# Kernel optimization log

Hardware: AMD Instinct MI355X
Metric: run time of the kernel (lower is better)

## Reference

```python
import jax, jax.numpy as jnp
import numpy as np

EPS = 1e-6
WEIGHTS = (1.0, 1.0, 1.0)  # (w_t, w_v, w_a)


def setup_inputs() -> dict:
    key = jax.random.key(0)
    k1, k2 = jax.random.split(key)
    B = 512
    similarity_cube = jax.random.normal(k1, (B, B, B), dtype=jnp.float32)
    target = jax.random.normal(k2, (B, 1), dtype=jnp.float32)
    return {"similarity_cube": similarity_cube, "target": target}


def reference(similarity_cube, target):
    # dataset == 'mosi' branch; reduction == 'mean'; weights == (1,1,1)
    # classes: round(target), >=0 -> 3, <0 -> -3 (never 0, so the eq-with-
    # intersection trick reduces to a pure 3-way class-equality mask)
    c = jnp.where(jnp.round(target[:, 0]) >= 0.0, 3.0, -3.0)  # (B,)
    # mask[i, j, k] = (c[j] == c[k]) & (c[j] == c[i])
    mask = ((c[None, :, None] == c[None, None, :])
            & (c[None, :, None] == c[:, None, None])).astype(similarity_cube.dtype)

    def axis_loss(axis):
        # masked NLL over one axis of the cube; denominators clamped at eps
        ls = jax.nn.log_softmax(similarity_cube, axis=axis)
        num = -jnp.sum(ls * mask, axis=axis)
        den = jnp.maximum(jnp.sum(mask, axis=axis), EPS)
        return num / den  # (B, B)

    # loss_t: softmax over dim 1 (transpose(1,2).view) -> per-(i,k)
    # loss_v: softmax over dim 2 (plain view)          -> per-(i,j)
    # loss_a: softmax over dim 0 (permute(1,2,0).view) -> per-(j,k)
    # all three are (B,B) row-major flattenings, so elementwise add matches torch
    loss = (WEIGHTS[0] * axis_loss(1)
            + WEIGHTS[1] * axis_loss(2)
            + WEIGHTS[2] * axis_loss(0))
    return jnp.mean(loss)
```

## Files before the change

kernel.cpp:

```cpp
#include <hip/hip_runtime.h>
#include <math.h>

#define Bn 512


__global__ void prep_kernel(const float* __restrict__ target,
                            int* __restrict__ cls,
                            int* __restrict__ nplus,
                            float* __restrict__ acc) {
    __shared__ int cnt;
    const int t = threadIdx.x;
    if (t == 0) cnt = 0;
    __syncthreads();
    const int c = (rintf(target[t]) >= 0.0f) ? 1 : 0;
    cls[t] = c;
    atomicAdd(&cnt, c);
    __syncthreads();
    if (t == 0) { *nplus = cnt; *acc = 0.0f; }
}

__global__ __launch_bounds__(256) void conloss_main(
    const float* __restrict__ cube,
    const int* __restrict__ cls,
    const int* __restrict__ nplus_p,
    float* __restrict__ acc)
{
    __shared__ int   sc[Bn];
    __shared__ float sE[4][Bn];
    __shared__ float sS[4][Bn];
    __shared__ float sred[256];

    const int tid = threadIdx.x;
    for (int t = tid; t < Bn; t += 256) sc[t] = cls[t];
    __syncthreads();
    const int np = *nplus_p;
    const int bid = blockIdx.x;
    float total = 0.0f;

    if (bid < Bn) {
        const int i = bid;
        const int ci = sc[i];
        const float inv_ng = 1.0f / (float)(ci ? np : (Bn - np));
        const int wave = tid >> 6;
        const int lane = tid & 63;
        const float* slice = cube + (size_t)i * (size_t)(Bn * Bn);
        const int ka = 4 * lane;
        const int kb = 256 + 4 * lane;

        float4 km_a, km_b;
        km_a.x = (sc[ka+0] == ci) ? 1.0f : 0.0f;
        km_a.y = (sc[ka+1] == ci) ? 1.0f : 0.0f;
        km_a.z = (sc[ka+2] == ci) ? 1.0f : 0.0f;
        km_a.w = (sc[ka+3] == ci) ? 1.0f : 0.0f;
        km_b.x = (sc[kb+0] == ci) ? 1.0f : 0.0f;
        km_b.y = (sc[kb+1] == ci) ? 1.0f : 0.0f;
        km_b.z = (sc[kb+2] == ci) ? 1.0f : 0.0f;
        km_b.w = (sc[kb+3] == ci) ? 1.0f : 0.0f;

        float4 cE_a = make_float4(0.f,0.f,0.f,0.f), cE_b = make_float4(0.f,0.f,0.f,0.f);
        float4 cS_a = make_float4(0.f,0.f,0.f,0.f), cS_b = make_float4(0.f,0.f,0.f,0.f);

        for (int j = wave; j < Bn; j += 4) {
            const float* row = slice + (size_t)j * Bn;
            const float4 xa = *(const float4*)(row + ka);
            const float4 xb = *(const float4*)(row + kb);
            float4 ea, eb;
            ea.x = __expf(xa.x); ea.y = __expf(xa.y); ea.z = __expf(xa.z); ea.w = __expf(xa.w);
            eb.x = __expf(xb.x); eb.y = __expf(xb.y); eb.z = __expf(xb.z); eb.w = __expf(xb.w);

            const float jm = (sc[j] == ci) ? 1.0f : 0.0f;
            cE_a.x += ea.x; cE_a.y += ea.y; cE_a.z += ea.z; cE_a.w += ea.w;
            cE_b.x += eb.x; cE_b.y += eb.y; cE_b.z += eb.z; cE_b.w += eb.w;
            cS_a.x += jm * xa.x; cS_a.y += jm * xa.y; cS_a.z += jm * xa.z; cS_a.w += jm * xa.w;
            cS_b.x += jm * xb.x; cS_b.y += jm * xb.y; cS_b.z += jm * xb.z; cS_b.w += jm * xb.w;

            float rE = ((ea.x + ea.y) + (ea.z + ea.w)) + ((eb.x + eb.y) + (eb.z + eb.w));
            float rS = km_a.x * xa.x + km_a.y * xa.y + km_a.z * xa.z + km_a.w * xa.w
                     + km_b.x * xb.x + km_b.y * xb.y + km_b.z * xb.z + km_b.w * xb.w;
            #pragma unroll
            for (int off = 32; off > 0; off >>= 1) {
                rE += __shfl_xor(rE, off, 64);
                rS += __shfl_xor(rS, off, 64);
            }
            if (lane == 0) {
                total += jm * (__logf(rE) - rS * inv_ng);
            }
        }

        sE[wave][ka+0] = cE_a.x; sE[wave][ka+1] = cE_a.y; sE[wave][ka+2] = cE_a.z; sE[wave][ka+3] = cE_a.w;
        sE[wave][kb+0] = cE_b.x; sE[wave][kb+1] = cE_b.y; sE[wave][kb+2] = cE_b.z; sE[wave][kb+3] = cE_b.w;
        sS[wave][ka+0] = cS_a.x; sS[wave][ka+1] = cS_a.y; sS[wave][ka+2] = cS_a.z; sS[wave][ka+3] = cS_a.w;
        sS[wave][kb+0] = cS_b.x; sS[wave][kb+1] = cS_b.y; sS[wave][kb+2] = cS_b.z; sS[wave][kb+3] = cS_b.w;
        __syncthreads();
        for (int k = tid; k < Bn; k += 256) {
            const float ce = (sE[0][k] + sE[1][k]) + (sE[2][k] + sE[3][k]);
            const float cs = (sS[0][k] + sS[1][k]) + (sS[2][k] + sS[3][k]);
            const float m = (sc[k] == ci) ? 1.0f : 0.0f;
            total += m * (__logf(ce) - cs * inv_ng);
        }
    } else {
        const int j = bid - Bn;
        const int cj = sc[j];
        const float inv_ng = 1.0f / (float)(cj ? np : (Bn - np));
        const float* base = cube + (size_t)j * Bn;
        const int k0 = 2 * tid;
        float2 E = make_float2(0.f, 0.f), S = make_float2(0.f, 0.f);
        #pragma unroll 8
        for (int ii = 0; ii < Bn; ++ii) {
            const float2 x = *(const float2*)(base + (size_t)ii * (size_t)(Bn * Bn) + k0);
            const float im = (sc[ii] == cj) ? 1.0f : 0.0f;
            E.x += __expf(x.x); E.y += __expf(x.y);
            S.x += im * x.x;    S.y += im * x.y;
        }
        const float m0 = (sc[k0]   == cj) ? 1.0f : 0.0f;
        const float m1 = (sc[k0+1] == cj) ? 1.0f : 0.0f;
        total += m0 * (__logf(E.x) - S.x * inv_ng);
        total += m1 * (__logf(E.y) - S.y * inv_ng);
    }

    sred[tid] = total;
    __syncthreads();
    for (int s = 128; s > 0; s >>= 1) {
        if (tid < s) sred[tid] += sred[tid + s];
        __syncthreads();
    }
    if (tid == 0) atomicAdd(acc, sred[0]);
}

__global__ void finalize_kernel(const float* __restrict__ acc, float* __restrict__ out) {
    out[0] = acc[0] * (1.0f / ((float)Bn * (float)Bn));
}

extern "C" void kernel_launch(void* const* d_in, const int* in_sizes, int n_in,
                              void* d_out, int out_size, void* d_ws, size_t ws_size,
                              hipStream_t stream) {
    const float* cube   = (const float*)d_in[0];
    const float* target = (const float*)d_in[1];
    float* out = (float*)d_out;

    float* acc   = (float*)d_ws;
    int*   nplus = (int*)d_ws + 1;
    int*   cls   = (int*)d_ws + 16;

    prep_kernel<<<1, Bn, 0, stream>>>(target, cls, nplus, acc);
    conloss_main<<<2 * Bn, 256, 0, stream>>>(cube, cls, nplus, acc);
    finalize_kernel<<<1, 1, 0, stream>>>(acc, out);
}
```

Baseline: 752.7 us.

## Interleave block types, use nontemporal float4 loads, split axis-0 pass across halves

Even and odd blocks now alternate between the slice-wise pass (axes 1/2) and the strided axis-0 pass, so both kinds of work run on the GPU at the same time instead of in two phases. All cube loads use nontemporal float4 loads to avoid polluting cache. The axis-0 blocks now use float4 loads and split the 512 slices between two thread halves, combining the halves through shared memory. This trades an extra sync and shared-memory step for wider loads and better concurrency, against a memory-bound read of the cube that happens twice.

```diff
diff --git a/kernel.cpp b/kernel.cpp
--- a/kernel.cpp
+++ b/kernel.cpp
@@ -3,6 +3,13 @@
 
 #define Bn 512
 
+typedef float fx4 __attribute__((ext_vector_type(4)));
+
+
+__device__ __forceinline__ float4 ntload4(const float* p) {
+    fx4 v = __builtin_nontemporal_load((const fx4*)p);
+    return make_float4(v.x, v.y, v.z, v.w);
+}
 
 __global__ void prep_kernel(const float* __restrict__ target,
                             int* __restrict__ cls,
@@ -37,8 +44,8 @@
     const int bid = blockIdx.x;
     float total = 0.0f;
 
-    if (bid < Bn) {
-        const int i = bid;
+    if ((bid & 1) == 0) {
+        const int i = bid >> 1;
         const int ci = sc[i];
         const float inv_ng = 1.0f / (float)(ci ? np : (Bn - np));
         const int wave = tid >> 6;
@@ -62,8 +69,8 @@
 
         for (int j = wave; j < Bn; j += 4) {
             const float* row = slice + (size_t)j * Bn;
-            const float4 xa = *(const float4*)(row + ka);
-            const float4 xb = *(const float4*)(row + kb);
+            const float4 xa = ntload4(row + ka);
+            const float4 xb = ntload4(row + kb);
             float4 ea, eb;
             ea.x = __expf(xa.x); ea.y = __expf(xa.y); ea.z = __expf(xa.z); ea.w = __expf(xa.w);
             eb.x = __expf(xb.x); eb.y = __expf(xb.y); eb.z = __expf(xb.z); eb.w = __expf(xb.w);
@@ -99,23 +106,36 @@
             total += m * (__logf(ce) - cs * inv_ng);
         }
     } else {
-        const int j = bid - Bn;
+        const int j = bid >> 1;
         const int cj = sc[j];
         const float inv_ng = 1.0f / (float)(cj ? np : (Bn - np));
         const float* base = cube + (size_t)j * Bn;
-        const int k0 = 2 * tid;
-        float2 E = make_float2(0.f, 0.f), S = make_float2(0.f, 0.f);
+        const int half = tid >> 7;
+        const int t    = tid & 127;
+        const int k0 = 4 * t;
+        float4 E = make_float4(0.f,0.f,0.f,0.f);
+        float4 S = make_float4(0.f,0.f,0.f,0.f);
         #pragma unroll 8
-        for (int ii = 0; ii < Bn; ++ii) {
-            const float2 x = *(const float2*)(base + (size_t)ii * (size_t)(Bn * Bn) + k0);
-            const float im = (sc[ii] == cj) ? 1.0f : 0.0f;
-            E.x += __expf(x.x); E.y += __expf(x.y);
-            S.x += im * x.x;    S.y += im * x.y;
+        for (int ii = 0; ii < Bn / 2; ++ii) {
+            const int s = 2 * ii + half;
+            const float4 x = ntload4(base + (size_t)s * (size_t)(Bn * Bn) + k0);
+            const float im = (sc[s] == cj) ? 1.0f : 0.0f;
+            E.x += __expf(x.x); E.y += __expf(x.y); E.z += __expf(x.z); E.w += __expf(x.w);
+            S.x += im * x.x;    S.y += im * x.y;    S.z += im * x.z;    S.w += im * x.w;
         }
-        const float m0 = (sc[k0]   == cj) ? 1.0f : 0.0f;
-        const float m1 = (sc[k0+1] == cj) ? 1.0f : 0.0f;
-        total += m0 * (__logf(E.x) - S.x * inv_ng);
-        total += m1 * (__logf(E.y) - S.y * inv_ng);
+        sE[half][k0+0] = E.x; sE[half][k0+1] = E.y; sE[half][k0+2] = E.z; sE[half][k0+3] = E.w;
+        sS[half][k0+0] = S.x; sS[half][k0+1] = S.y; sS[half][k0+2] = S.z; sS[half][k0+3] = S.w;
+        __syncthreads();
+        if (half == 0) {
+            #pragma unroll
+            for (int q = 0; q < 4; ++q) {
+                const int k = k0 + q;
+                const float e = sE[0][k] + sE[1][k];
+                const float s = sS[0][k] + sS[1][k];
+                const float m = (sc[k] == cj) ? 1.0f : 0.0f;
+                total += m * (__logf(e) - s * inv_ng);
+            }
+        }
     }
 
     sred[tid] = total;
```

Measured after the change: 730.5 us. 1.03x faster.
